# Kernel optimization log

Hardware: AMD Instinct MI355X
Metric: run time of the kernel (lower is better)

## Reference

```python
import jax, jax.numpy as jnp
import numpy as np

N_NODES = 100000
IN_FEATURES = 5000
OUT_FEATURES = 64
NNZ = 4000000


def setup_inputs() -> dict:
    key = jax.random.key(0)
    k_row, k_col, k_val, k_w, k_b = jax.random.split(key, 5)
    rows = jax.random.randint(k_row, (NNZ,), 0, N_NODES, dtype=jnp.int64 if jax.config.jax_enable_x64 else jnp.int32)
    cols = jax.random.randint(k_col, (NNZ,), 0, IN_FEATURES, dtype=rows.dtype)
    index = jnp.stack([rows, cols], axis=0)  # [2, nnz] COO
    value = jax.random.uniform(k_val, (NNZ,), dtype=jnp.float32)
    # kaiming_uniform_(mode='fan_out', a=sqrt(5)) on [in, out]: fan_out = out_features
    gain = np.sqrt(2.0 / (1.0 + 5.0))
    bound_w = gain * np.sqrt(3.0 / OUT_FEATURES)
    weight = jax.random.uniform(k_w, (IN_FEATURES, OUT_FEATURES), jnp.float32, -bound_w, bound_w)
    bound_b = 1.0 / np.sqrt(OUT_FEATURES)
    bias = jax.random.uniform(k_b, (OUT_FEATURES,), jnp.float32, -bound_b, bound_b)
    return {"index": index, "value": value, "n": N_NODES, "weight": weight, "bias": bias}


def reference(index, value, n, weight, bias):
    # spmm: out[r, :] = sum over nnz with row==r of value * weight[col, :]
    rows, cols = index[0], index[1]
    contrib = value[:, None] * weight[cols]            # [nnz, out] gather + scale
    res = jax.ops.segment_sum(contrib, rows, num_segments=n)  # [n, out] scatter-add
    return res + bias[None, :]
```

## Files before the change

kernel.cpp:

```cpp
#include <hip/hip_runtime.h>


#define NBF 1024
#define DMAX 128
#define CH 4096
#define CC 1536
#define SP_T 512

__global__ void k_zero1024(int* __restrict__ p) { p[threadIdx.x] = 0; }

__global__ __launch_bounds__(512) void kA_hist(const int* __restrict__ rows, int nnz,
        unsigned M, int S, int* __restrict__ hist2dF, int* __restrict__ hist2dC) {
    __shared__ int h[NBF];
    int t = threadIdx.x, blk = blockIdx.x;
    long long base = (long long)blk * CH;
    int count = (int)min((long long)CH, (long long)nnz - base);
    h[t] = 0; h[t + 512] = 0;
    __syncthreads();
#pragma unroll
    for (int k = 0; k < 8; ++k) {
        int i = t + (k << 9);
        if (i < count) {
            unsigned r = (unsigned)rows[base + i];
            int f = (int)(((unsigned long long)r * M) >> S);
            atomicAdd(&h[f], 1);
        }
    }
    __syncthreads();
    hist2dF[blk * NBF + t] = h[t];
    hist2dF[blk * NBF + 512 + t] = h[t + 512];
    if (t < 64) {
        int s = 0;
#pragma unroll
        for (int j = 0; j < 16; ++j) s += h[(t << 4) + j];
        hist2dC[(blk << 6) + t] = s;
    }
}

__global__ __launch_bounds__(1024) void kB1_reduce(const int* __restrict__ hist2dF,
        int nChunks, int* __restrict__ gcnt) {
    int t = threadIdx.x;
    int s = 0;
    for (int b = blockIdx.x; b < nChunks; b += gridDim.x) s += hist2dF[b * NBF + t];
    if (s) atomicAdd(&gcnt[t], s);
}

__global__ __launch_bounds__(1024) void kB_off(const int* __restrict__ gcnt,
        const int* __restrict__ hist2dC, int nChunks, int* __restrict__ fineBase,
        int* __restrict__ cursorF, int* __restrict__ blockOffC, int doOff) {
    __shared__ int sE[NBF];
    __shared__ int wsum[16];
    __shared__ int totalSh;
    int t = threadIdx.x, lane = t & 63, wv = t >> 6;
    int v = gcnt[t];
    int x = v;
#pragma unroll
    for (int off = 1; off < 64; off <<= 1) {
        int y = __shfl_up(x, off, 64);
        if (lane >= off) x += y;
    }
    if (lane == 63) wsum[wv] = x;
    __syncthreads();
    if (t < 16) {
        int s = wsum[t], xs = s;
#pragma unroll
        for (int off = 1; off < 16; off <<= 1) {
            int y = __shfl_up(xs, off, 16);
            if (t >= off) xs += y;
        }
        wsum[t] = xs - s;
    }
    __syncthreads();
    int incl = x + wsum[wv], excl = incl - v;
    sE[t] = excl;
    if (blockIdx.x == 0) {
        fineBase[t] = excl;
        cursorF[t] = excl;
        if (t == NBF - 1) fineBase[NBF] = incl;
    }
    __syncthreads();
    if (!doOff) return;
    int c = blockIdx.x;
    int carry = sE[c << 4];
    for (int b2 = 0; b2 < nChunks; b2 += 1024) {
        int idx = b2 + t;
        int hv = (idx < nChunks) ? hist2dC[(idx << 6) + c] : 0;
        int hx = hv;
#pragma unroll
        for (int off = 1; off < 64; off <<= 1) {
            int y = __shfl_up(hx, off, 64);
            if (lane >= off) hx += y;
        }
        if (lane == 63) wsum[wv] = hx;
        __syncthreads();
        if (t < 16) {
            int s = wsum[t], xs = s;
#pragma unroll
            for (int off = 1; off < 16; off <<= 1) {
                int y = __shfl_up(xs, off, 16);
                if (t >= off) xs += y;
            }
            wsum[t] = xs - s;
        }
        __syncthreads();
        int hincl = hx + wsum[wv];
        if (idx < nChunks) blockOffC[(idx << 6) + c] = carry + hincl - hv;
        if (t == 1023) totalSh = hincl;
        __syncthreads();
        carry += totalSh;
    }
}

__global__ void k_ghist(const int* __restrict__ rows, int nnz, unsigned M, int S,
                        int* __restrict__ gcnt) {
    __shared__ int h[NBF];
    int t = threadIdx.x;
    for (int i = t; i < NBF; i += blockDim.x) h[i] = 0;
    __syncthreads();
    for (int i = blockIdx.x * blockDim.x + t; i < nnz; i += gridDim.x * blockDim.x) {
        unsigned r = (unsigned)rows[i];
        int f = (int)(((unsigned long long)r * M) >> S);
        atomicAdd(&h[f], 1);
    }
    __syncthreads();
    for (int i = t; i < NBF; i += blockDim.x)
        if (h[i]) atomicAdd(&gcnt[i], h[i]);
}

__global__ __launch_bounds__(512) void kC_bin1(const int* __restrict__ rows,
        const int* __restrict__ cols, const float* __restrict__ vals, int nnz,
        unsigned M, int S, int d, const int* __restrict__ blockOffC,
        unsigned long long* __restrict__ pairs1) {
    __shared__ unsigned long long stage[CH];
    __shared__ int histC[64], scC[64], adjC[64];
    int t = threadIdx.x, blk = blockIdx.x;
    long long base = (long long)blk * CH;
    int count = (int)min((long long)CH, (long long)nnz - base);
    if (t < 64) histC[t] = 0;
    __syncthreads();
    int cs8[8], rk8[8];
    unsigned long long pk8[8];
#pragma unroll
    for (int k = 0; k < 8; ++k) {
        int i = t + (k << 9);
        cs8[k] = -1;
        if (i < count) {
            unsigned r = (unsigned)rows[base + i];
            int c = cols[base + i];
            float v = vals[base + i];
            int f = (int)(((unsigned long long)r * M) >> S);
            int lr = (int)r - f * d;
            int cs = f >> 4;
            cs8[k] = cs;
            rk8[k] = atomicAdd(&histC[cs], 1);
            pk8[k] = ((unsigned long long)__float_as_uint(v) << 32) |
                     ((unsigned)f << 20) | ((unsigned)lr << 13) | (unsigned)c;
        }
    }
    __syncthreads();
    if (t < 64) {
        int v = histC[t], x = v;
#pragma unroll
        for (int off = 1; off < 64; off <<= 1) {
            int y = __shfl_up(x, off, 64);
            if (t >= off) x += y;
        }
        scC[t] = x;
        adjC[t] = blockOffC[(blk << 6) + t] - (x - v);
    }
    __syncthreads();
#pragma unroll
    for (int k = 0; k < 8; ++k)
        if (cs8[k] >= 0) stage[(scC[cs8[k]] - histC[cs8[k]]) + rk8[k]] = pk8[k];
    __syncthreads();
    for (int i = t; i < count; i += 512) {
        unsigned long long p = stage[i];
        int cs = (int)((p >> 24) & 63);
        pairs1[adjC[cs] + i] = p;
    }
}

__global__ __launch_bounds__(1024) void kD_bin2(const unsigned long long* __restrict__ pairs1,
        int nnz, int* __restrict__ cursorF, unsigned long long* __restrict__ pairs2) {
    __shared__ unsigned long long stage[CH];
    __shared__ int histW[64], scW[64], adjW[64];
    __shared__ int f0sh;
    int t = threadIdx.x;
    long long base = (long long)blockIdx.x * CH;
    int count = (int)min((long long)CH, (long long)nnz - base);
    if (t == 0) {
        int fFirst = (int)((pairs1[base] >> 20) & 1023);
        int fLast  = (int)((pairs1[base + count - 1] >> 20) & 1023);
        int f0 = (fFirst >> 4) << 4;
        f0sh = (fLast < f0 + 64) ? f0 : -1;
    }
    if (t < 64) histW[t] = 0;
    __syncthreads();
    int f0 = f0sh;
    if (f0 < 0) {
#pragma unroll
        for (int k = 0; k < 4; ++k) {
            int i = t + (k << 10);
            if (i < count) {
                unsigned long long p = pairs1[base + i];
                int f = (int)((p >> 20) & 1023);
                int pos = atomicAdd(&cursorF[f], 1);
                pairs2[pos] = p;
            }
        }
        return;
    }
    int k4[4], rk4[4];
    unsigned long long pk4[4];
#pragma unroll
    for (int k = 0; k < 4; ++k) {
        int i = t + (k << 10);
        k4[k] = -1;
        if (i < count) {
            unsigned long long p = pairs1[base + i];
            int kf = (int)((p >> 20) & 1023) - f0;
            k4[k] = kf;
            rk4[k] = atomicAdd(&histW[kf], 1);
            pk4[k] = p;
        }
    }
    __syncthreads();
    if (t < 64) {
        int v = histW[t], x = v;
#pragma unroll
        for (int off = 1; off < 64; off <<= 1) {
            int y = __shfl_up(x, off, 64);
            if (t >= off) x += y;
        }
        scW[t] = x;
        if (v > 0) {
            int g = atomicAdd(&cursorF[f0 + t], v);
            adjW[t] = g - (x - v);
        }
    }
    __syncthreads();
#pragma unroll
    for (int k = 0; k < 4; ++k)
        if (k4[k] >= 0) stage[(scW[k4[k]] - histW[k4[k]]) + rk4[k]] = pk4[k];
    __syncthreads();
    for (int i = t; i < count; i += 1024) {
        unsigned long long p = stage[i];
        int kf = (int)((p >> 20) & 1023) - f0;
        pairs2[adjW[kf] + i] = p;
    }
}

__global__ __launch_bounds__(1024) void k_bin_direct(const int* __restrict__ rows,
        const int* __restrict__ cols, const float* __restrict__ vals, int nnz,
        unsigned M, int S, int d, int* __restrict__ cursorF,
        unsigned long long* __restrict__ pairs1) {
    __shared__ unsigned long long stage[CH];
    __shared__ int histF[NBF], scF[NBF], adjF[NBF];
    __shared__ int wsum[16];
    int t = threadIdx.x, lane = t & 63, wv = t >> 6;
    long long base = (long long)blockIdx.x * CH;
    int count = (int)min((long long)CH, (long long)nnz - base);
    histF[t] = 0;
    __syncthreads();
    int f4[4], rk4[4];
    unsigned long long pk4[4];
#pragma unroll
    for (int k = 0; k < 4; ++k) {
        int i = t + (k << 10);
        f4[k] = -1;
        if (i < count) {
            unsigned r = (unsigned)rows[base + i];
            int c = cols[base + i];
            float vv = vals[base + i];
            int f = (int)(((unsigned long long)r * M) >> S);
            int lr = (int)r - f * d;
            f4[k] = f;
            rk4[k] = atomicAdd(&histF[f], 1);
            pk4[k] = ((unsigned long long)__float_as_uint(vv) << 32) |
                     ((unsigned)f << 20) | ((unsigned)lr << 13) | (unsigned)c;
        }
    }
    __syncthreads();
    int v = histF[t], x = v;
#pragma unroll
    for (int off = 1; off < 64; off <<= 1) {
        int y = __shfl_up(x, off, 64);
        if (lane >= off) x += y;
    }
    if (lane == 63) wsum[wv] = x;
    __syncthreads();
    if (t < 16) {
        int s = wsum[t], xs = s;
#pragma unroll
        for (int off = 1; off < 16; off <<= 1) {
            int y = __shfl_up(xs, off, 16);
            if (t >= off) xs += y;
        }
        wsum[t] = xs - s;
    }
    __syncthreads();
    int incl = x + wsum[wv];
    scF[t] = incl;
    if (v > 0) {
        int g = atomicAdd(&cursorF[t], v);
        adjF[t] = g - (incl - v);
    }
    __syncthreads();
#pragma unroll
    for (int k = 0; k < 4; ++k)
        if (f4[k] >= 0) stage[(scF[f4[k]] - histF[f4[k]]) + rk4[k]] = pk4[k];
    __syncthreads();
    for (int i = t; i < count; i += 1024) {
        unsigned long long p = stage[i];
        int f = (int)((p >> 20) & 1023);
        pairs1[adjF[f] + i] = p;
    }
}

__global__ __launch_bounds__(SP_T, 8) void k_spmm5(
        const unsigned long long* __restrict__ pairs, const int* __restrict__ fineBase,
        const float* __restrict__ weight, const float* __restrict__ bias,
        float* __restrict__ out, int d, int n) {
    __shared__ unsigned long long stage[CC];
    __shared__ int histR[DMAX], scR[DMAX];
    extern __shared__ float acc[];
    int b = blockIdx.x, t = threadIdx.x;
    int row0 = b * d;
    if (row0 >= n) return;
    int nrows = min(d, n - row0);
    int start = fineBase[b], end = fineBase[b + 1];

    for (int i = t; i < (nrows << 6); i += SP_T) acc[i] = 0.0f;

    int g = t >> 4, fq = t & 15;
    for (int cb = start; cb < end; cb += CC) {
        int cnt = min(CC, end - cb);
        if (t < DMAX) histR[t] = 0;
        __syncthreads();
        int lr3[3], rk3[3];
        unsigned long long pk3[3];
#pragma unroll
        for (int k = 0; k < 3; ++k) {
            int i = t + (k << 9);
            lr3[k] = -1;
            if (i < cnt) {
                unsigned long long p = pairs[cb + i];
                int lr = (int)((p >> 13) & 127);
                lr3[k] = lr;
                rk3[k] = atomicAdd(&histR[lr], 1);
                pk3[k] = p;
            }
        }
        __syncthreads();
        if (t < DMAX) {
            int v = histR[t], x = v;
            int lane = t & 63;
#pragma unroll
            for (int off = 1; off < 64; off <<= 1) {
                int y = __shfl_up(x, off, 64);
                if (lane >= off) x += y;
            }
            scR[t] = x;
        }
        __syncthreads();
        if (t >= 64 && t < DMAX) scR[t] += scR[63];
        __syncthreads();
#pragma unroll
        for (int k = 0; k < 3; ++k)
            if (lr3[k] >= 0) stage[(scR[lr3[k]] - histR[lr3[k]]) + rk3[k]] = pk3[k];
        __syncthreads();

        for (int r = g; r < nrows; r += 32) {
            int e = scR[r], s = e - histR[r];
            if (s >= e) continue;
            float4 a = {0.0f, 0.0f, 0.0f, 0.0f};
            int j = s;
            for (; j + 4 <= e; j += 4) {
                unsigned long long p0 = stage[j + 0];
                unsigned long long p1 = stage[j + 1];
                unsigned long long p2 = stage[j + 2];
                unsigned long long p3 = stage[j + 3];
                const float4 w0 = *(const float4*)(weight + (((int)(p0 & 8191)) << 6) + (fq << 2));
                const float4 w1 = *(const float4*)(weight + (((int)(p1 & 8191)) << 6) + (fq << 2));
                const float4 w2 = *(const float4*)(weight + (((int)(p2 & 8191)) << 6) + (fq << 2));
                const float4 w3 = *(const float4*)(weight + (((int)(p3 & 8191)) << 6) + (fq << 2));
                float v0 = __uint_as_float((unsigned)(p0 >> 32));
                float v1 = __uint_as_float((unsigned)(p1 >> 32));
                float v2 = __uint_as_float((unsigned)(p2 >> 32));
                float v3 = __uint_as_float((unsigned)(p3 >> 32));
                a.x = fmaf(v0, w0.x, a.x); a.y = fmaf(v0, w0.y, a.y);
                a.z = fmaf(v0, w0.z, a.z); a.w = fmaf(v0, w0.w, a.w);
                a.x = fmaf(v1, w1.x, a.x); a.y = fmaf(v1, w1.y, a.y);
                a.z = fmaf(v1, w1.z, a.z); a.w = fmaf(v1, w1.w, a.w);
                a.x = fmaf(v2, w2.x, a.x); a.y = fmaf(v2, w2.y, a.y);
                a.z = fmaf(v2, w2.z, a.z); a.w = fmaf(v2, w2.w, a.w);
                a.x = fmaf(v3, w3.x, a.x); a.y = fmaf(v3, w3.y, a.y);
                a.z = fmaf(v3, w3.z, a.z); a.w = fmaf(v3, w3.w, a.w);
            }
            for (; j < e; ++j) {
                unsigned long long p = stage[j];
                float vv = __uint_as_float((unsigned)(p >> 32));
                const float4 w = *(const float4*)(weight + (((int)(p & 8191)) << 6) + (fq << 2));
                a.x = fmaf(vv, w.x, a.x); a.y = fmaf(vv, w.y, a.y);
                a.z = fmaf(vv, w.z, a.z); a.w = fmaf(vv, w.w, a.w);
            }
            float4* ap = (float4*)&acc[(r << 6) + (fq << 2)];
            float4 o = *ap;
            o.x += a.x; o.y += a.y; o.z += a.z; o.w += a.w;
            *ap = o;
        }
        __syncthreads();
    }

    for (int i = t; i < (nrows << 6); i += SP_T)
        out[((long long)row0 << 6) + i] = acc[i] + bias[i & 63];
}

extern "C" void kernel_launch(void* const* d_in, const int* in_sizes, int n_in,
                              void* d_out, int out_size, void* d_ws, size_t ws_size,
                              hipStream_t stream) {
    const int*   index  = (const int*)d_in[0];
    const float* value  = (const float*)d_in[1];
    const float* weight = (const float*)d_in[3];
    const float* bias   = (const float*)d_in[4];
    float*       out    = (float*)d_out;

    int nnz = in_sizes[0] / 2;
    int n   = out_size / 64;
    const int* rows = index;
    const int* cols = index + nnz;

    int d = (n + NBF - 1) / NBF;
    unsigned M = 0;
    int S = 0;
    for (S = 20; S <= 40; ++S) {
        unsigned long long m = ((1ull << S) + (unsigned)d - 1) / (unsigned)d;
        unsigned long long e = m * (unsigned long long)d - (1ull << S);
        if (m <= 0xffffffffull && e * (unsigned long long)(n > 0 ? n - 1 : 0) < (1ull << S)) {
            M = (unsigned)m;
            break;
        }
    }

    int nChunks = (nnz + CH - 1) / CH;
    char* ws = (char*)d_ws;
    int* fineBase = (int*)ws;
    int* cursorF  = (int*)(ws + (8 << 10));
    int* gcnt     = (int*)(ws + (12 << 10));
    size_t offC = 64 << 10;
    size_t szC  = (((size_t)nChunks * 64 * 4) + 255) & ~(size_t)255;
    size_t offO = offC + szC;
    size_t offF = offO + szC;
    size_t szF  = (((size_t)nChunks * NBF * 4) + 255) & ~(size_t)255;
    size_t offP1 = offF + szF;
    size_t szP   = (((size_t)nnz * 8) + 255) & ~(size_t)255;
    size_t offP2 = offP1 + szP;
    int* hist2dC   = (int*)(ws + offC);
    int* blockOffC = (int*)(ws + offO);
    int* hist2dF   = (int*)(ws + offF);
    unsigned long long* pairs1 = (unsigned long long*)(ws + offP1);
    unsigned long long* pairs2 = (unsigned long long*)(ws + offP2);
    unsigned long long* pairs3 = (unsigned long long*)(ws + offC);

    bool two = ws_size >= offP2 + szP;
    bool dir = !two && ws_size >= offP1 + szP;

    k_zero1024<<<1, 1024, 0, stream>>>(gcnt);
    size_t smem = (size_t)d * 64 * sizeof(float);
    if (two || dir) {
        kA_hist<<<nChunks, 512, 0, stream>>>(rows, nnz, M, S, hist2dF, hist2dC);
        kB1_reduce<<<64, 1024, 0, stream>>>(hist2dF, nChunks, gcnt);
        if (two) {
            kB_off<<<64, 1024, 0, stream>>>(gcnt, hist2dC, nChunks, fineBase, cursorF,
                                            blockOffC, 1);
            kC_bin1<<<nChunks, 512, 0, stream>>>(rows, cols, value, nnz, M, S, d,
                                                 blockOffC, pairs1);
            kD_bin2<<<nChunks, 1024, 0, stream>>>(pairs1, nnz, cursorF, pairs2);
            k_spmm5<<<NBF, SP_T, smem, stream>>>(pairs2, fineBase, weight, bias, out, d, n);
        } else {
            kB_off<<<1, 1024, 0, stream>>>(gcnt, hist2dC, nChunks, fineBase, cursorF,
                                           blockOffC, 0);
            k_bin_direct<<<nChunks, 1024, 0, stream>>>(rows, cols, value, nnz, M, S, d,
                                                       cursorF, pairs1);
            k_spmm5<<<NBF, SP_T, smem, stream>>>(pairs1, fineBase, weight, bias, out, d, n);
        }
    } else {
        k_ghist<<<256, 512, 0, stream>>>(rows, nnz, M, S, gcnt);
        kB_off<<<1, 1024, 0, stream>>>(gcnt, hist2dC, nChunks, fineBase, cursorF,
                                       blockOffC, 0);
        k_bin_direct<<<nChunks, 1024, 0, stream>>>(rows, cols, value, nnz, M, S, d,
                                                   cursorF, pairs3);
        k_spmm5<<<NBF, SP_T, smem, stream>>>(pairs3, fineBase, weight, bias, out, d, n);
    }
}
```

Baseline: 186.7 us.

## Drop two-pass binning in favor of single direct atomic binning pass

Removes the two-level radix binning path (per-chunk histograms, coarse bin pass, fine bin pass) and always uses the global histogram plus a single direct-binning kernel writing into one pairs buffer. The goal is fewer kernel launches and one less full read/write pass over the 4M packed pairs. The cost is more global atomic contention on the fine-bin cursors and less coalesced scatter writes in the direct binning kernel.

```diff
diff --git a/kernel.cpp b/kernel.cpp
--- a/kernel.cpp
+++ b/kernel.cpp
@@ -9,40 +9,20 @@
 
 __global__ void k_zero1024(int* __restrict__ p) { p[threadIdx.x] = 0; }
 
-__global__ __launch_bounds__(512) void kA_hist(const int* __restrict__ rows, int nnz,
-        unsigned M, int S, int* __restrict__ hist2dF, int* __restrict__ hist2dC) {
+__global__ void k_ghist(const int* __restrict__ rows, int nnz, unsigned M, int S,
+                        int* __restrict__ gcnt) {
     __shared__ int h[NBF];
-    int t = threadIdx.x, blk = blockIdx.x;
-    long long base = (long long)blk * CH;
-    int count = (int)min((long long)CH, (long long)nnz - base);
-    h[t] = 0; h[t + 512] = 0;
-    __syncthreads();
-#pragma unroll
-    for (int k = 0; k < 8; ++k) {
-        int i = t + (k << 9);
-        if (i < count) {
-            unsigned r = (unsigned)rows[base + i];
-            int f = (int)(((unsigned long long)r * M) >> S);
-            atomicAdd(&h[f], 1);
-        }
-    }
-    __syncthreads();
-    hist2dF[blk * NBF + t] = h[t];
-    hist2dF[blk * NBF + 512 + t] = h[t + 512];
-    if (t < 64) {
-        int s = 0;
-#pragma unroll
-        for (int j = 0; j < 16; ++j) s += h[(t << 4) + j];
-        hist2dC[(blk << 6) + t] = s;
-    }
-}
-
-__global__ __launch_bounds__(1024) void kB1_reduce(const int* __restrict__ hist2dF,
-        int nChunks, int* __restrict__ gcnt) {
     int t = threadIdx.x;
-    int s = 0;
-    for (int b = blockIdx.x; b < nChunks; b += gridDim.x) s += hist2dF[b * NBF + t];
-    if (s) atomicAdd(&gcnt[t], s);
+    for (int i = t; i < NBF; i += blockDim.x) h[i] = 0;
+    __syncthreads();
+    for (int i = blockIdx.x * blockDim.x + t; i < nnz; i += gridDim.x * blockDim.x) {
+        unsigned r = (unsigned)rows[i];
+        int f = (int)(((unsigned long long)r * M) >> S);
+        atomicAdd(&h[f], 1);
+    }
+    __syncthreads();
+    for (int i = t; i < NBF; i += blockDim.x)
+        if (h[i]) atomicAdd(&gcnt[i], h[i]);
 }
 
 __global__ __launch_bounds__(1024) void kB_off(const int* __restrict__ gcnt,
@@ -108,145 +88,6 @@
         if (t == 1023) totalSh = hincl;
         __syncthreads();
         carry += totalSh;
-    }
-}
-
-__global__ void k_ghist(const int* __restrict__ rows, int nnz, unsigned M, int S,
-                        int* __restrict__ gcnt) {
-    __shared__ int h[NBF];
-    int t = threadIdx.x;
-    for (int i = t; i < NBF; i += blockDim.x) h[i] = 0;
-    __syncthreads();
-    for (int i = blockIdx.x * blockDim.x + t; i < nnz; i += gridDim.x * blockDim.x) {
-        unsigned r = (unsigned)rows[i];
-        int f = (int)(((unsigned long long)r * M) >> S);
-        atomicAdd(&h[f], 1);
-    }
-    __syncthreads();
-    for (int i = t; i < NBF; i += blockDim.x)
-        if (h[i]) atomicAdd(&gcnt[i], h[i]);
-}
-
-__global__ __launch_bounds__(512) void kC_bin1(const int* __restrict__ rows,
-        const int* __restrict__ cols, const float* __restrict__ vals, int nnz,
-        unsigned M, int S, int d, const int* __restrict__ blockOffC,
-        unsigned long long* __restrict__ pairs1) {
-    __shared__ unsigned long long stage[CH];
-    __shared__ int histC[64], scC[64], adjC[64];
-    int t = threadIdx.x, blk = blockIdx.x;
-    long long base = (long long)blk * CH;
-    int count = (int)min((long long)CH, (long long)nnz - base);
-    if (t < 64) histC[t] = 0;
-    __syncthreads();
-    int cs8[8], rk8[8];
-    unsigned long long pk8[8];
-#pragma unroll
-    for (int k = 0; k < 8; ++k) {
-        int i = t + (k << 9);
-        cs8[k] = -1;
-        if (i < count) {
-            unsigned r = (unsigned)rows[base + i];
-            int c = cols[base + i];
-            float v = vals[base + i];
-            int f = (int)(((unsigned long long)r * M) >> S);
-            int lr = (int)r - f * d;
-            int cs = f >> 4;
-            cs8[k] = cs;
-            rk8[k] = atomicAdd(&histC[cs], 1);
-            pk8[k] = ((unsigned long long)__float_as_uint(v) << 32) |
-                     ((unsigned)f << 20) | ((unsigned)lr << 13) | (unsigned)c;
-        }
-    }
-    __syncthreads();
-    if (t < 64) {
-        int v = histC[t], x = v;
-#pragma unroll
-        for (int off = 1; off < 64; off <<= 1) {
-            int y = __shfl_up(x, off, 64);
-            if (t >= off) x += y;
-        }
-        scC[t] = x;
-        adjC[t] = blockOffC[(blk << 6) + t] - (x - v);
-    }
-    __syncthreads();
-#pragma unroll
-    for (int k = 0; k < 8; ++k)
-        if (cs8[k] >= 0) stage[(scC[cs8[k]] - histC[cs8[k]]) + rk8[k]] = pk8[k];
-    __syncthreads();
-    for (int i = t; i < count; i += 512) {
-        unsigned long long p = stage[i];
-        int cs = (int)((p >> 24) & 63);
-        pairs1[adjC[cs] + i] = p;
-    }
-}
-
-__global__ __launch_bounds__(1024) void kD_bin2(const unsigned long long* __restrict__ pairs1,
-        int nnz, int* __restrict__ cursorF, unsigned long long* __restrict__ pairs2) {
-    __shared__ unsigned long long stage[CH];
-    __shared__ int histW[64], scW[64], adjW[64];
-    __shared__ int f0sh;
-    int t = threadIdx.x;
-    long long base = (long long)blockIdx.x * CH;
-    int count = (int)min((long long)CH, (long long)nnz - base);
-    if (t == 0) {
-        int fFirst = (int)((pairs1[base] >> 20) & 1023);
-        int fLast  = (int)((pairs1[base + count - 1] >> 20) & 1023);
-        int f0 = (fFirst >> 4) << 4;
-        f0sh = (fLast < f0 + 64) ? f0 : -1;
-    }
-    if (t < 64) histW[t] = 0;
-    __syncthreads();
-    int f0 = f0sh;
-    if (f0 < 0) {
-#pragma unroll
-        for (int k = 0; k < 4; ++k) {
-            int i = t + (k << 10);
-            if (i < count) {
-                unsigned long long p = pairs1[base + i];
-                int f = (int)((p >> 20) & 1023);
-                int pos = atomicAdd(&cursorF[f], 1);
-                pairs2[pos] = p;
-            }
-        }
-        return;
-    }
-    int k4[4], rk4[4];
-    unsigned long long pk4[4];
-#pragma unroll
-    for (int k = 0; k < 4; ++k) {
-        int i = t + (k << 10);
-        k4[k] = -1;
-        if (i < count) {
-            unsigned long long p = pairs1[base + i];
-            int kf = (int)((p >> 20) & 1023) - f0;
-            k4[k] = kf;
-            rk4[k] = atomicAdd(&histW[kf], 1);
-            pk4[k] = p;
-        }
-    }
-    __syncthreads();
-    if (t < 64) {
-        int v = histW[t], x = v;
-#pragma unroll
-        for (int off = 1; off < 64; off <<= 1) {
-            int y = __shfl_up(x, off, 64);
-            if (t >= off) x += y;
-        }
-        scW[t] = x;
-        if (v > 0) {
-            int g = atomicAdd(&cursorF[f0 + t], v);
-            adjW[t] = g - (x - v);
-        }
-    }
-    __syncthreads();
-#pragma unroll
-    for (int k = 0; k < 4; ++k)
-        if (k4[k] >= 0) stage[(scW[k4[k]] - histW[k4[k]]) + rk4[k]] = pk4[k];
-    __syncthreads();
-    for (int i = t; i < count; i += 1024) {
-        unsigned long long p = stage[i];
-        int kf = (int)((p >> 20) & 1023) - f0;
-        pairs2[adjW[kf] + i] = p;
     }
 }
 
@@ -454,42 +295,20 @@
     size_t szF  = (((size_t)nChunks * NBF * 4) + 255) & ~(size_t)255;
     size_t offP1 = offF + szF;
     size_t szP   = (((size_t)nnz * 8) + 255) & ~(size_t)255;
-    size_t offP2 = offP1 + szP;
     int* hist2dC   = (int*)(ws + offC);
     int* blockOffC = (int*)(ws + offO);
-    int* hist2dF   = (int*)(ws + offF);
     unsigned long long* pairs1 = (unsigned long long*)(ws + offP1);
-    unsigned long long* pairs2 = (unsigned long long*)(ws + offP2);
     unsigned long long* pairs3 = (unsigned long long*)(ws + offC);
 
-    bool two = ws_size >= offP2 + szP;
-    bool dir = !two && ws_size >= offP1 + szP;
+    bool fits = ws_size >= offP1 + szP;
+    unsigned long long* pairs = fits ? pairs1 : pairs3;
 
     k_zero1024<<<1, 1024, 0, stream>>>(gcnt);
     size_t smem = (size_t)d * 64 * sizeof(float);
-    if (two || dir) {
-        kA_hist<<<nChunks, 512, 0, stream>>>(rows, nnz, M, S, hist2dF, hist2dC);
-        kB1_reduce<<<64, 1024, 0, stream>>>(hist2dF, nChunks, gcnt);
-        if (two) {
-            kB_off<<<64, 1024, 0, stream>>>(gcnt, hist2dC, nChunks, fineBase, cursorF,
-                                            blockOffC, 1);
-            kC_bin1<<<nChunks, 512, 0, stream>>>(rows, cols, value, nnz, M, S, d,
-                                                 blockOffC, pairs1);
-            kD_bin2<<<nChunks, 1024, 0, stream>>>(pairs1, nnz, cursorF, pairs2);
-            k_spmm5<<<NBF, SP_T, smem, stream>>>(pairs2, fineBase, weight, bias, out, d, n);
-        } else {
-            kB_off<<<1, 1024, 0, stream>>>(gcnt, hist2dC, nChunks, fineBase, cursorF,
-                                           blockOffC, 0);
-            k_bin_direct<<<nChunks, 1024, 0, stream>>>(rows, cols, value, nnz, M, S, d,
-                                                       cursorF, pairs1);
-            k_spmm5<<<NBF, SP_T, smem, stream>>>(pairs1, fineBase, weight, bias, out, d, n);
-        }
-    } else {
-        k_ghist<<<256, 512, 0, stream>>>(rows, nnz, M, S, gcnt);
-        kB_off<<<1, 1024, 0, stream>>>(gcnt, hist2dC, nChunks, fineBase, cursorF,
-                                       blockOffC, 0);
-        k_bin_direct<<<nChunks, 1024, 0, stream>>>(rows, cols, value, nnz, M, S, d,
-                                                   cursorF, pairs3);
-        k_spmm5<<<NBF, SP_T, smem, stream>>>(pairs3, fineBase, weight, bias, out, d, n);
-    }
-}
+    k_ghist<<<256, 512, 0, stream>>>(rows, nnz, M, S, gcnt);
+    kB_off<<<1, 1024, 0, stream>>>(gcnt, hist2dC, nChunks, fineBase, cursorF,
+                                   blockOffC, 0);
+    k_bin_direct<<<nChunks, 1024, 0, stream>>>(rows, cols, value, nnz, M, S, d,
+                                               cursorF, pairs);
+    k_spmm5<<<NBF, SP_T, smem, stream>>>(pairs, fineBase, weight, bias, out, d, n);
+}
```

Measured after the change: 195.6 us. +4.8%, slower.
